# Kernel optimization log

Measured on AMD Instinct MI355X. Metric: run time of the kernel, lower is better.

## Reference

```python
import jax, jax.numpy as jnp
import numpy as np

B, T, C = 4, 2048, 1024
H = 16
D = C // H  # head_dim = 64
SCALE = D ** -0.5


def setup_inputs() -> dict:
    key = jax.random.key(0)
    ks = jax.random.split(key, 5)
    x = jax.random.normal(ks[0], (B, T, C), dtype=jnp.float32)
    w_qkv = jax.random.normal(ks[1], (3 * C, C), dtype=jnp.float32) * (C ** -0.5)
    b_qkv = jnp.zeros((3 * C,), dtype=jnp.float32)
    w_proj = jax.random.normal(ks[2], (C, C), dtype=jnp.float32) * (C ** -0.5)
    b_proj = jnp.zeros((C,), dtype=jnp.float32)
    return {"x": x, "w_qkv": w_qkv, "b_qkv": b_qkv, "w_proj": w_proj, "b_proj": b_proj}


def reference(x, w_qkv, b_qkv, w_proj, b_proj):
    b, t, c = x.shape
    # fused qkv projection (torch Linear: x @ W.T + b)
    qkv = x @ w_qkv.T + b_qkv                      # [B, T, 3C]
    q, k, v = jnp.split(qkv, 3, axis=2)
    # [B, T, C] -> [B, H, T, D]
    q = q.reshape(b, t, H, D).transpose(0, 2, 1, 3)
    k = k.reshape(b, t, H, D).transpose(0, 2, 1, 3)
    v = v.reshape(b, t, H, D).transpose(0, 2, 1, 3)
    att = jnp.einsum('bhqd,bhkd->bhqk', q, k) * SCALE
    causal = jnp.tril(jnp.ones((t, t), dtype=bool))  # True = keep
    att = jnp.where(causal, att, -jnp.inf)
    att = jax.nn.softmax(att, axis=-1)
    out = jnp.einsum('bhqk,bhkd->bhqd', att, v)
    out = out.transpose(0, 2, 1, 3).reshape(b, t, c)
    return out @ w_proj.T + b_proj
```

## Files before the change

kernel.cpp:

```cpp
#include <hip/hip_runtime.h>

typedef unsigned short u16;
typedef __attribute__((ext_vector_type(8))) short short8;
typedef __attribute__((ext_vector_type(4))) float f32x4;
typedef __attribute__((ext_vector_type(16))) float f32x16;
typedef __attribute__((ext_vector_type(2))) unsigned uint2v;
typedef __attribute__((ext_vector_type(4))) unsigned u32x4;

#define AS1 __attribute__((address_space(1)))
#define AS3 __attribute__((address_space(3)))

constexpr int Bn = 4, Tn = 2048, Cn = 1024, Hn = 16, Dn = 64;
constexpr float SCL_LOG2E = 0.125f * 1.44269504088896f;

__device__ __forceinline__ u16 f2bf(float f) {
  union { float f; unsigned u; } v; v.f = f;
  unsigned r = v.u + 0x7FFFu + ((v.u >> 16) & 1u);
  return (u16)(r >> 16);
}

__device__ __forceinline__ unsigned cvtpk_bf16(float a, float b) {
  unsigned r;
  asm("v_cvt_pk_bf16_f32 %0, %1, %2" : "=v"(r) : "v"(a), "v"(b));
  return r;
}

__global__ void cast_f32_to_bf16(const float* __restrict__ in, u16* __restrict__ out, int n4) {
  int i = blockIdx.x * 256 + threadIdx.x;
  if (i >= n4) return;
  float4 v = ((const float4*)in)[i];
  ushort4 o;
  o.x = f2bf(v.x); o.y = f2bf(v.y); o.z = f2bf(v.z); o.w = f2bf(v.w);
  ((ushort4*)out)[i] = o;
}

__device__ __forceinline__ void store_out(u16* p, float v) { *p = f2bf(v); }
__device__ __forceinline__ void store_out(float* p, float v) { *p = v; }

template <typename OT>
__global__ __launch_bounds__(512) void gemm8(
    const u16* __restrict__ A, const u16* __restrict__ Bm,
    const float* __restrict__ bias, OT* __restrict__ C,
    int M, int N, int K, int nbn, int qcols, float qscale)
{
  __shared__ u16 As[2][128 * 64];
  __shared__ u16 Bs[2][2][128 * 64];

  const int tid = threadIdx.x;
  const int lane = tid & 63;
  const int w = tid >> 6;
  const int wm = w >> 2, wn = w & 3;
  const int l15 = lane & 15, lg = lane >> 4;

  const int nwg = gridDim.x;
  const int wg = (blockIdx.x & 7) * (nwg >> 3) + (blockIdx.x >> 3);
  const int m0 = (wg / nbn) * 128;
  const int n0 = (wg % nbn) * 256;
  const int NT = K >> 6;

  const int wrow = wm * 64;

  f32x4 acc[4][4] = {};

  auto stage_A = [&](int tt) {
    if (tt >= NT) return;
    const int bu = tt & 1;
#pragma unroll
    for (int it = 0; it < 2; ++it) {
      const int c = it * 512 + tid;
      const int row = c >> 3;
      const int cs = (c & 7) ^ (row & 7);
      const u16* g = A + (size_t)(m0 + row) * K + tt * 64 + cs * 8;
      __builtin_amdgcn_global_load_lds((const AS1 void*)g,
          (AS3 void*)(&As[bu][c * 8]), 16, 0, 0);
    }
  };
  auto stage_B = [&](int tt, int h) {
    if (tt >= NT) return;
    const int bu = tt & 1;
#pragma unroll
    for (int it = 0; it < 2; ++it) {
      const int c = it * 512 + tid;
      const int i = c >> 3;
      const int cs = (c & 7) ^ (i & 7);
      const int grow = n0 + ((i >> 5) << 6) + (h << 5) + (i & 31);
      const u16* g = Bm + (size_t)grow * K + tt * 64 + cs * 8;
      __builtin_amdgcn_global_load_lds((const AS1 void*)g,
          (AS3 void*)(&Bs[bu][h][c * 8]), 16, 0, 0);
    }
  };

  auto readA = [&](int bu, int mh, short8 (*a)[2]) {
#pragma unroll
    for (int i = 0; i < 2; ++i)
#pragma unroll
      for (int ks = 0; ks < 2; ++ks) {
        const int ra = wrow + (mh * 2 + i) * 16 + l15;
        a[i][ks] = *(const short8*)(&As[bu][ra * 64 + (((ks * 4 + lg) ^ (ra & 7)) << 3)]);
      }
  };
  auto readB = [&](int bu, int nh, short8 (*b)[2]) {
#pragma unroll
    for (int j = 0; j < 2; ++j)
#pragma unroll
      for (int ks = 0; ks < 2; ++ks) {
        const int i = wn * 32 + j * 16 + l15;
        b[j][ks] = *(const short8*)(&Bs[bu][nh][i * 64 + (((ks * 4 + lg) ^ (i & 7)) << 3)]);
      }
  };
  auto mmaq = [&](int mh, int nh, short8 (*a)[2], short8 (*b)[2]) {
    __builtin_amdgcn_s_setprio(1);
#pragma unroll
    for (int i = 0; i < 2; ++i)
#pragma unroll
      for (int j = 0; j < 2; ++j)
#pragma unroll
        for (int ks = 0; ks < 2; ++ks)
          acc[mh * 2 + i][nh * 2 + j] = __builtin_amdgcn_mfma_f32_16x16x32_bf16(
              a[i][ks], b[j][ks], acc[mh * 2 + i][nh * 2 + j], 0, 0, 0);
    __builtin_amdgcn_s_setprio(0);
  };

  stage_A(0);
  stage_B(0, 0);
  stage_B(0, 1);
  stage_A(1);
  asm volatile("s_waitcnt vmcnt(4)" ::: "memory");
  __builtin_amdgcn_sched_barrier(0);
  __builtin_amdgcn_s_barrier();

  for (int t = 0; t < NT; ++t) {
    const int bu = t & 1;
    short8 a0[2][2], a1[2][2], b0[2][2], b1[2][2];
    readA(bu, 0, a0);
    readB(bu, 0, b0);
    stage_B(t + 1, 0);
    __builtin_amdgcn_s_barrier();
    mmaq(0, 0, a0, b0);
    if (t + 1 < NT) asm volatile("s_waitcnt vmcnt(4)" ::: "memory");
    else            asm volatile("s_waitcnt vmcnt(0)" ::: "memory");
    __builtin_amdgcn_sched_barrier(0);
    __builtin_amdgcn_s_barrier();
    readB(bu, 1, b1);
    stage_B(t + 1, 1);
    __builtin_amdgcn_s_barrier();
    mmaq(0, 1, a0, b1);
    __builtin_amdgcn_s_barrier();
    readA(bu, 1, a1);
    __builtin_amdgcn_s_barrier();
    mmaq(1, 1, a1, b1);
    __builtin_amdgcn_s_barrier();
    stage_A(t + 2);
    __builtin_amdgcn_s_barrier();
    mmaq(1, 0, a1, b0);
    if (t + 2 < NT) {
      asm volatile("s_waitcnt vmcnt(4)" ::: "memory");
      __builtin_amdgcn_sched_barrier(0);
    } else if (t + 1 < NT) {
      asm volatile("s_waitcnt vmcnt(2)" ::: "memory");
      __builtin_amdgcn_sched_barrier(0);
    }
    __builtin_amdgcn_s_barrier();
  }

#pragma unroll
  for (int i = 0; i < 4; ++i) {
    const int rowg = m0 + wrow + i * 16 + lg * 4;
#pragma unroll
    for (int j = 0; j < 4; ++j) {
      const int colg = n0 + wn * 64 + j * 16 + l15;
      const float sc = (colg < qcols) ? qscale : 1.0f;
      const float bv = bias[colg];
#pragma unroll
      for (int r = 0; r < 4; ++r)
        store_out(C + (size_t)(rowg + r) * N + colg, (acc[i][j][r] + bv) * sc);
    }
  }
}

__global__ __launch_bounds__(256) void transpose_v(
    const u16* __restrict__ qkv, u16* __restrict__ vt)
{
  __shared__ u16 tile[64][72];
  const int bh = blockIdx.x >> 5;
  const int tt = blockIdx.x & 31;
  const int b = bh >> 4;
  const int h = bh & 15;
  const int tid = threadIdx.x;
  const int trow = tid >> 2;
  const int dseg = tid & 3;

  const u16* src = qkv + (size_t)(b * Tn + tt * 64 + trow) * (3 * Cn) + 2 * Cn + h * Dn + dseg * 16;
  short8 v0 = *(const short8*)src;
  short8 v1 = *(const short8*)(src + 8);
#pragma unroll
  for (int e = 0; e < 8; ++e) {
    tile[dseg * 16 + e][trow] = (u16)v0[e];
    tile[dseg * 16 + 8 + e][trow] = (u16)v1[e];
  }
  __syncthreads();

  const int drow = tid >> 2;
  const int tseg = tid & 3;
  u16* dst = vt + (size_t)(bh * Dn + drow) * Tn + tt * 64 + tseg * 16;
  *(short8*)dst = *(const short8*)&tile[drow][tseg * 16];
  *(short8*)(dst + 8) = *(const short8*)&tile[drow][tseg * 16 + 8];
}

__global__ __launch_bounds__(256) void attn_kernel(
    const u16* __restrict__ qkv, const u16* __restrict__ vt, u16* __restrict__ att)
{
  __shared__ u16 Ks[2][64 * 64];
  __shared__ u16 Vs[2][64 * 64];
  const int tid = threadIdx.x;
  const int lane = tid & 63;
  const int w = tid >> 6;
  const int l31 = lane & 31;
  const int hi = lane >> 5;

  const int blk = blockIdx.x;
  const int qt = (Tn / 128 - 1) - (blk >> 6);
  const int bh = blk & 63;
  const int b = bh >> 4;
  const int h = bh & 15;
  const int q0w = qt * 128 + w * 32;
  const int rowbase = b * Tn;
  const int koff = Cn + h * Dn;
  const size_t vbase = (size_t)bh * Dn * Tn;
  const int nt = 2 * qt + 2;
  const int ntw = 2 * qt + 1 + (w >> 1);

  short8 qf[4];
  {
    const u16* qp = qkv + (size_t)(rowbase + q0w + l31) * (3 * Cn) + h * Dn + hi * 8;
#pragma unroll
    for (int sub = 0; sub < 4; ++sub) qf[sub] = *(const short8*)(qp + sub * 16);
  }

  float m_r = -1e30f, l_r = 0.f;
  f32x16 oacc[2] = {};

#define STAGE(buf, t_)                                                            \
  {                                                                               \
    const int kt_ = (t_) * 64;                                                    \
    _Pragma("unroll")                                                             \
    for (int it = 0; it < 2; ++it) {                                              \
      int c = it * 256 + tid;                                                     \
      int row = c >> 3;                                                           \
      int cs = (c & 7) ^ (row & 7);                                               \
      const u16* gk = qkv + (size_t)(rowbase + kt_ + row) * (3 * Cn) + koff + cs * 8; \
      __builtin_amdgcn_global_load_lds((const AS1 void*)gk, (AS3 void*)(&Ks[buf][c * 8]), 16, 0, 0); \
      const u16* gv = vt + vbase + (size_t)row * Tn + kt_ + cs * 8;               \
      __builtin_amdgcn_global_load_lds((const AS1 void*)gv, (AS3 void*)(&Vs[buf][c * 8]), 16, 0, 0); \
    }                                                                             \
  }

  STAGE(0, 0);
  __syncthreads();

  for (int t = 0; t < nt; ++t) {
    const int cur = t & 1;
    if (t + 1 < nt) STAGE(cur ^ 1, t + 1);
    if (t < ntw) {
      const int kt = t * 64;
      const u16* Kb = Ks[cur];
      const u16* Vb = Vs[cur];

      f32x16 s0 = {}, s1 = {};
#pragma unroll
      for (int sub = 0; sub < 4; ++sub) {
        const int ch = sub * 2 + hi;
        const int r0 = l31;
        short8 kf0 = *(const short8*)(Kb + r0 * 64 + ((ch ^ (r0 & 7)) << 3));
        s0 = __builtin_amdgcn_mfma_f32_32x32x16_bf16(kf0, qf[sub], s0, 0, 0, 0);
        const int r1 = 32 + l31;
        short8 kf1 = *(const short8*)(Kb + r1 * 64 + ((ch ^ (r1 & 7)) << 3));
        s1 = __builtin_amdgcn_mfma_f32_32x32x16_bf16(kf1, qf[sub], s1, 0, 0, 0);
      }

      if (kt + 63 > q0w) {
        const int qa = q0w + l31;
#pragma unroll
        for (int r = 0; r < 16; ++r) {
          const int k0 = kt + ((r & 3) + 8 * (r >> 2)) + 4 * hi;
          if (k0 > qa) s0[r] = -1e30f;
          if (k0 + 32 > qa) s1[r] = -1e30f;
        }
      }

      float mx = s0[0];
#pragma unroll
      for (int r = 1; r < 16; ++r) mx = fmaxf(mx, s0[r]);
#pragma unroll
      for (int r = 0; r < 16; ++r) mx = fmaxf(mx, s1[r]);
      mx = fmaxf(mx, __shfl_xor(mx, 32));

      if (__any(mx > m_r + 8.f)) {
        const float mnew = fmaxf(m_r, mx);
        const float a = __builtin_amdgcn_exp2f(m_r - mnew);
        m_r = mnew;
        l_r *= a;
#pragma unroll
        for (int r = 0; r < 16; ++r) { oacc[0][r] *= a; oacc[1][r] *= a; }
      }

      float ps = 0.f;
#pragma unroll
      for (int r = 0; r < 16; ++r) {
        s0[r] = __builtin_amdgcn_exp2f(s0[r] - m_r); ps += s0[r];
        s1[r] = __builtin_amdgcn_exp2f(s1[r] - m_r); ps += s1[r];
      }
      ps += __shfl_xor(ps, 32);
      l_r += ps;

      short8 pfr[4];
#pragma unroll
      for (int ks = 0; ks < 4; ++ks) {
        const f32x16& sv = (ks < 2) ? s0 : s1;
        const int base = (ks & 1) * 8;
        unsigned a0 = cvtpk_bf16(sv[base + 0], sv[base + 1]);
        unsigned a1 = cvtpk_bf16(sv[base + 2], sv[base + 3]);
        unsigned b0 = cvtpk_bf16(sv[base + 4], sv[base + 5]);
        unsigned b1 = cvtpk_bf16(sv[base + 6], sv[base + 7]);
        uint2v s_0 = __builtin_amdgcn_permlane32_swap(a0, b0, false, false);
        uint2v s_1 = __builtin_amdgcn_permlane32_swap(a1, b1, false, false);
        union { u32x4 u; short8 s; } cvt;
        cvt.u = (u32x4){s_0.x, s_1.x, s_0.y, s_1.y};
        pfr[ks] = cvt.s;
      }

#pragma unroll
      for (int j = 0; j < 2; ++j) {
        const int rv = j * 32 + l31;
        const int rsw = (rv & 7) << 3;
#pragma unroll
        for (int ks = 0; ks < 4; ++ks) {
          short8 vf = *(const short8*)(Vb + rv * 64 + (((ks * 2 + hi) << 3) ^ rsw));
          oacc[j] = __builtin_amdgcn_mfma_f32_32x32x16_bf16(vf, pfr[ks], oacc[j], 0, 0, 0);
        }
      }
    }
    __syncthreads();
  }

  {
    const float inv = __builtin_amdgcn_rcpf(l_r);
    u16* orow = att + (size_t)(rowbase + q0w + l31) * Cn + h * Dn + hi * 4;
#pragma unroll
    for (int j = 0; j < 2; ++j)
#pragma unroll
      for (int g = 0; g < 4; ++g) {
        ushort4 o;
#pragma unroll
        for (int c = 0; c < 4; ++c) o[c] = f2bf(oacc[j][g * 4 + c] * inv);
        *(ushort4*)(orow + j * 32 + g * 8) = o;
      }
  }
#undef STAGE
}

extern "C" void kernel_launch(void* const* d_in, const int* in_sizes, int n_in,
                              void* d_out, int out_size, void* d_ws, size_t ws_size,
                              hipStream_t stream) {
  const float* x      = (const float*)d_in[0];
  const float* w_qkv  = (const float*)d_in[1];
  const float* b_qkv  = (const float*)d_in[2];
  const float* w_proj = (const float*)d_in[3];
  const float* b_proj = (const float*)d_in[4];
  float* out = (float*)d_out;

  char* ws = (char*)d_ws;
  u16* x_bf     = (u16*)(ws);
  u16* wqkv_bf  = (u16*)(ws + 16777216);
  u16* wproj_bf = (u16*)(ws + 16777216 + 6291456);
  u16* qkv      = (u16*)(ws + 25165824);
  u16* att      = (u16*)(ws + 75497472);
  u16* vt       = x_bf;

  const int M = Bn * Tn;

  cast_f32_to_bf16<<<(M * Cn / 4 + 255) / 256, 256, 0, stream>>>(x, x_bf, M * Cn / 4);
  cast_f32_to_bf16<<<(3 * Cn * Cn / 4 + 255) / 256, 256, 0, stream>>>(w_qkv, wqkv_bf, 3 * Cn * Cn / 4);
  cast_f32_to_bf16<<<(Cn * Cn / 4 + 255) / 256, 256, 0, stream>>>(w_proj, wproj_bf, Cn * Cn / 4);

  gemm8<u16><<<768, 512, 0, stream>>>(
      x_bf, wqkv_bf, b_qkv, qkv, M, 3 * Cn, Cn, 12, Cn, SCL_LOG2E);

  transpose_v<<<Bn * Hn * (Tn / 64), 256, 0, stream>>>(qkv, vt);

  attn_kernel<<<Bn * Hn * (Tn / 128), 256, 0, stream>>>(qkv, vt, att);

  gemm8<float><<<256, 512, 0, stream>>>(
      att, wproj_bf, b_proj, out, M, Cn, Cn, 4, 0, 1.0f);
}
```

Measured before the change: 176.5 us.

## Shrink GEMM tile to 128x128 and stage epilogue through LDS for coalesced stores

Changes the GEMM block tile from 128x256 to 128x128, halving B staging and per-wave accumulators, and doubles the grid for both projection GEMMs to raise occupancy and workgroup count. The epilogue now writes results into LDS and then emits vectorized, coalesced global stores instead of scattered scalar stores. The cost is lower arithmetic intensity per tile and more total global traffic for A, plus extra barriers in the epilogue.

```diff
diff --git a/kernel.cpp b/kernel.cpp
--- a/kernel.cpp
+++ b/kernel.cpp
@@ -34,9 +34,6 @@
   ((ushort4*)out)[i] = o;
 }
 
-__device__ __forceinline__ void store_out(u16* p, float v) { *p = f2bf(v); }
-__device__ __forceinline__ void store_out(float* p, float v) { *p = v; }
-
 template <typename OT>
 __global__ __launch_bounds__(512) void gemm8(
     const u16* __restrict__ A, const u16* __restrict__ Bm,
@@ -44,7 +41,7 @@
     int M, int N, int K, int nbn, int qcols, float qscale)
 {
   __shared__ u16 As[2][128 * 64];
-  __shared__ u16 Bs[2][2][128 * 64];
+  __shared__ u16 Bs[2][128 * 64];
 
   const int tid = threadIdx.x;
   const int lane = tid & 63;
@@ -55,12 +52,13 @@
   const int nwg = gridDim.x;
   const int wg = (blockIdx.x & 7) * (nwg >> 3) + (blockIdx.x >> 3);
   const int m0 = (wg / nbn) * 128;
-  const int n0 = (wg % nbn) * 256;
+  const int n0 = (wg % nbn) * 128;
   const int NT = K >> 6;
 
   const int wrow = wm * 64;
-
-  f32x4 acc[4][4] = {};
+  const int wcol = wn * 32;
+
+  f32x4 acc[4][2] = {};
 
   auto stage_A = [&](int tt) {
     if (tt >= NT) return;
@@ -75,18 +73,17 @@
           (AS3 void*)(&As[bu][c * 8]), 16, 0, 0);
     }
   };
-  auto stage_B = [&](int tt, int h) {
+  auto stage_B = [&](int tt) {
     if (tt >= NT) return;
     const int bu = tt & 1;
 #pragma unroll
     for (int it = 0; it < 2; ++it) {
       const int c = it * 512 + tid;
-      const int i = c >> 3;
-      const int cs = (c & 7) ^ (i & 7);
-      const int grow = n0 + ((i >> 5) << 6) + (h << 5) + (i & 31);
-      const u16* g = Bm + (size_t)grow * K + tt * 64 + cs * 8;
+      const int row = c >> 3;
+      const int cs = (c & 7) ^ (row & 7);
+      const u16* g = Bm + (size_t)(n0 + row) * K + tt * 64 + cs * 8;
       __builtin_amdgcn_global_load_lds((const AS1 void*)g,
-          (AS3 void*)(&Bs[bu][h][c * 8]), 16, 0, 0);
+          (AS3 void*)(&Bs[bu][c * 8]), 16, 0, 0);
     }
   };
 
@@ -101,48 +98,39 @@
   };
   auto readB = [&](int bu, int nh, short8 (*b)[2]) {
 #pragma unroll
-    for (int j = 0; j < 2; ++j)
-#pragma unroll
-      for (int ks = 0; ks < 2; ++ks) {
-        const int i = wn * 32 + j * 16 + l15;
-        b[j][ks] = *(const short8*)(&Bs[bu][nh][i * 64 + (((ks * 4 + lg) ^ (i & 7)) << 3)]);
-      }
+    for (int ks = 0; ks < 2; ++ks) {
+      const int rb = wcol + nh * 16 + l15;
+      b[0][ks] = *(const short8*)(&Bs[bu][rb * 64 + (((ks * 4 + lg) ^ (rb & 7)) << 3)]);
+    }
   };
   auto mmaq = [&](int mh, int nh, short8 (*a)[2], short8 (*b)[2]) {
     __builtin_amdgcn_s_setprio(1);
 #pragma unroll
     for (int i = 0; i < 2; ++i)
 #pragma unroll
-      for (int j = 0; j < 2; ++j)
-#pragma unroll
-        for (int ks = 0; ks < 2; ++ks)
-          acc[mh * 2 + i][nh * 2 + j] = __builtin_amdgcn_mfma_f32_16x16x32_bf16(
-              a[i][ks], b[j][ks], acc[mh * 2 + i][nh * 2 + j], 0, 0, 0);
+      for (int ks = 0; ks < 2; ++ks)
+        acc[mh * 2 + i][nh] = __builtin_amdgcn_mfma_f32_16x16x32_bf16(
+            a[i][ks], b[0][ks], acc[mh * 2 + i][nh], 0, 0, 0);
     __builtin_amdgcn_s_setprio(0);
   };
 
   stage_A(0);
-  stage_B(0, 0);
-  stage_B(0, 1);
+  stage_B(0);
   stage_A(1);
-  asm volatile("s_waitcnt vmcnt(4)" ::: "memory");
+  asm volatile("s_waitcnt vmcnt(2)" ::: "memory");
   __builtin_amdgcn_sched_barrier(0);
   __builtin_amdgcn_s_barrier();
 
   for (int t = 0; t < NT; ++t) {
     const int bu = t & 1;
-    short8 a0[2][2], a1[2][2], b0[2][2], b1[2][2];
+    short8 a0[2][2], a1[2][2], b0[1][2], b1[1][2];
     readA(bu, 0, a0);
     readB(bu, 0, b0);
-    stage_B(t + 1, 0);
+    stage_B(t + 1);
     __builtin_amdgcn_s_barrier();
     mmaq(0, 0, a0, b0);
-    if (t + 1 < NT) asm volatile("s_waitcnt vmcnt(4)" ::: "memory");
-    else            asm volatile("s_waitcnt vmcnt(0)" ::: "memory");
-    __builtin_amdgcn_sched_barrier(0);
     __builtin_amdgcn_s_barrier();
     readB(bu, 1, b1);
-    stage_B(t + 1, 1);
     __builtin_amdgcn_s_barrier();
     mmaq(0, 1, a0, b1);
     __builtin_amdgcn_s_barrier();
@@ -154,26 +142,64 @@
     __builtin_amdgcn_s_barrier();
     mmaq(1, 0, a1, b0);
     if (t + 2 < NT) {
-      asm volatile("s_waitcnt vmcnt(4)" ::: "memory");
+      asm volatile("s_waitcnt vmcnt(2)" ::: "memory");
       __builtin_amdgcn_sched_barrier(0);
     } else if (t + 1 < NT) {
-      asm volatile("s_waitcnt vmcnt(2)" ::: "memory");
+      asm volatile("s_waitcnt vmcnt(0)" ::: "memory");
       __builtin_amdgcn_sched_barrier(0);
     }
     __builtin_amdgcn_s_barrier();
   }
 
-#pragma unroll
-  for (int i = 0; i < 4; ++i) {
-    const int rowg = m0 + wrow + i * 16 + lg * 4;
-#pragma unroll
-    for (int j = 0; j < 4; ++j) {
-      const int colg = n0 + wn * 64 + j * 16 + l15;
-      const float sc = (colg < qcols) ? qscale : 1.0f;
-      const float bv = bias[colg];
-#pragma unroll
-      for (int r = 0; r < 4; ++r)
-        store_out(C + (size_t)(rowg + r) * N + colg, (acc[i][j][r] + bv) * sc);
+  __syncthreads();
+  if constexpr (__is_same(OT, u16)) {
+    u16* bounce = &As[0][0];
+#pragma unroll
+    for (int i = 0; i < 4; ++i)
+#pragma unroll
+      for (int j = 0; j < 2; ++j) {
+        const int colg = n0 + wcol + j * 16 + l15;
+        const float sc = (colg < qcols) ? qscale : 1.0f;
+        const float bv = bias[colg];
+#pragma unroll
+        for (int r = 0; r < 4; ++r)
+          bounce[(wrow + i * 16 + lg * 4 + r) * 128 + wcol + j * 16 + l15] =
+              f2bf((acc[i][j][r] + bv) * sc);
+      }
+    __syncthreads();
+#pragma unroll
+    for (int s = 0; s < 4; ++s) {
+      const int u = s * 512 + tid;
+      const int row = u >> 4, col = (u & 15) * 8;
+      *(short8*)(C + (size_t)(m0 + row) * N + n0 + col) =
+          *(const short8*)(&bounce[row * 128 + col]);
+    }
+  } else {
+    float* bounce = (float*)&As[0][0];
+#pragma unroll
+    for (int cch = 0; cch < 2; ++cch) {
+      if (wm == cch) {
+#pragma unroll
+        for (int i = 0; i < 4; ++i)
+#pragma unroll
+          for (int j = 0; j < 2; ++j) {
+            const int colg = n0 + wcol + j * 16 + l15;
+            const float bv = bias[colg];
+#pragma unroll
+            for (int r = 0; r < 4; ++r)
+              bounce[(i * 16 + lg * 4 + r) * 128 + wcol + j * 16 + l15] =
+                  acc[i][j][r] + bv;
+          }
+      }
+      __syncthreads();
+#pragma unroll
+      for (int s = 0; s < 4; ++s) {
+        const int u = s * 512 + tid;
+        const int row = u >> 5, col = (u & 31) * 4;
+        *(f32x4*)((float*)C + (size_t)(m0 + cch * 64 + row) * N + n0 + col) =
+            *(const f32x4*)(&bounce[row * 128 + col]);
+      }
+      __syncthreads();
     }
   }
 }
@@ -383,13 +409,13 @@
   cast_f32_to_bf16<<<(3 * Cn * Cn / 4 + 255) / 256, 256, 0, stream>>>(w_qkv, wqkv_bf, 3 * Cn * Cn / 4);
   cast_f32_to_bf16<<<(Cn * Cn / 4 + 255) / 256, 256, 0, stream>>>(w_proj, wproj_bf, Cn * Cn / 4);
 
-  gemm8<u16><<<768, 512, 0, stream>>>(
-      x_bf, wqkv_bf, b_qkv, qkv, M, 3 * Cn, Cn, 12, Cn, SCL_LOG2E);
+  gemm8<u16><<<1536, 512, 0, stream>>>(
+      x_bf, wqkv_bf, b_qkv, qkv, M, 3 * Cn, Cn, 24, Cn, SCL_LOG2E);
 
   transpose_v<<<Bn * Hn * (Tn / 64), 256, 0, stream>>>(qkv, vt);
 
   attn_kernel<<<Bn * Hn * (Tn / 128), 256, 0, stream>>>(qkv, vt, att);
 
-  gemm8<float><<<256, 512, 0, stream>>>(
-      att, wproj_bf, b_proj, out, M, Cn, Cn, 4, 0, 1.0f);
-}
+  gemm8<float><<<512, 512, 0, stream>>>(
+      att, wproj_bf, b_proj, out, M, Cn, Cn, 8, 0, 1.0f);
+}
```

Result: no change. 174.5 us (-1.1%).
